# Kernel optimization log

Hardware: AMD Instinct MI355X
Metric: run time of the kernel (lower is better)

The kernel has to match this reference:

```python
import jax, jax.numpy as jnp
import numpy as np

H = 256        # hidden_size
V = 8192       # output_size / vocab
S = 4096       # encoder source length


def _lin(x, w, b):
    # torch nn.Linear: x @ W^T + b, W shape [out, in]
    return x @ w.T + b


def setup_inputs() -> dict:
    key = jax.random.key(0)
    ks = jax.random.split(key, 32)
    f32 = jnp.float32

    def w(i, shape, scale=0.02):
        return (jax.random.normal(ks[i], shape) * scale).astype(f32)

    inp = {
        "input_tok": jax.random.randint(ks[0], (1,), 0, V),
        "hidden": jax.random.normal(ks[1], (1, H), dtype=f32),
        "encoder_outputs": jax.random.normal(ks[2], (S, 2 * H), dtype=f32),
        "emb": w(3, (V, V), 0.02),
        "Uz_w": w(4, (H, V)), "Uz_b": jnp.zeros((H,), f32),
        "Wz_w": w(5, (H, H)), "Wz_b": jnp.zeros((H,), f32),
        "Cz_w": w(6, (H, 2 * H)), "Cz_b": jnp.zeros((H,), f32),
        "Ur_w": w(7, (H, V)), "Ur_b": jnp.zeros((H,), f32),
        "Wr_w": w(8, (H, H)), "Wr_b": jnp.zeros((H,), f32),
        "Cr_w": w(9, (H, 2 * H)), "Cr_b": jnp.zeros((H,), f32),
        "Uh_w": w(10, (H, V)), "Uh_b": jnp.zeros((H,), f32),
        "Wh_w": w(11, (H, H)), "Wh_b": jnp.zeros((H,), f32),
        "Ch_w": w(12, (H, 2 * H)), "Ch_b": jnp.zeros((H,), f32),
        "Ua_w": w(13, (H, 2 * H)), "Ua_b": jnp.zeros((H,), f32),
        "Wa_w": w(14, (H, H)), "Wa_b": jnp.zeros((H,), f32),
        "Va_w": w(15, (1, H)), "Va_b": jnp.zeros((1,), f32),
        "V_w": w(16, (V, H)), "V_b": jnp.zeros((V,), f32),
    }
    return inp


def reference(input_tok, hidden, encoder_outputs, emb,
              Uz_w, Uz_b, Wz_w, Wz_b, Cz_w, Cz_b,
              Ur_w, Ur_b, Wr_w, Wr_b, Cr_w, Cr_b,
              Uh_w, Uh_b, Wh_w, Wh_b, Ch_w, Ch_b,
              Ua_w, Ua_b, Wa_w, Wa_b, Va_w, Va_b,
              V_w, V_b):
    y = emb[input_tok[0]].reshape(1, V)                                   # [1, V]
    # Bahdanau additive attention over encoder states (softmax over dim 0)
    e = jnp.tanh(_lin(hidden, Wa_w, Wa_b) + _lin(encoder_outputs, Ua_w, Ua_b))  # [S, H]
    Eij = _lin(e, Va_w, Va_b)                                             # [S, 1]
    aij = jax.nn.softmax(Eij, axis=0)                                     # [S, 1]
    Ci = jnp.sum(aij * encoder_outputs, axis=0).reshape(1, 2 * H)         # [1, 2H]
    # GRU gates
    z = jax.nn.sigmoid(_lin(y, Uz_w, Uz_b) + _lin(hidden, Wz_w, Wz_b) + _lin(Ci, Cz_w, Cz_b))
    r = jax.nn.sigmoid(_lin(y, Ur_w, Ur_b) + _lin(hidden, Wr_w, Wr_b) + _lin(Ci, Cr_w, Cr_b))
    c = jnp.tanh(_lin(y, Uh_w, Uh_b) + _lin(r * hidden, Wh_w, Wh_b) + _lin(Ci, Ch_w, Ch_b))
    hidden_new = (1.0 - z) * c + z * hidden                               # [1, H]
    out = jax.nn.log_softmax(_lin(hidden_new, V_w, V_b), axis=1)          # [1, V]
    return (out, hidden_new, aij)
```

## Files before the change

### kernel.cpp

```cpp
#include <hip/hip_runtime.h>
#include <hip/hip_bf16.h>

typedef unsigned short u16;
typedef unsigned int u32;

#define HD 256
#define VD 8192
#define SD 4096
#define H2 512

#define WS_FLAG  0
#define WS_WAH   64
#define WS_STATS 320
#define WS_CI    384
#define WS_G     896
#define WS_HN    1664
#define WS_EIJ   2048

__device__ __forceinline__ float bflo(u32 w) { return __uint_as_float(w << 16); }
__device__ __forceinline__ float bfhi(u32 w) { return __uint_as_float(w & 0xffff0000u); }
__device__ __forceinline__ float bfu(u16 u)  { return __uint_as_float(((u32)u) << 16); }

__device__ __forceinline__ float ldf(const void* p, long i, int bf) {
    return bf ? bfu(((const u16*)p)[i]) : ((const float*)p)[i];
}
__device__ __forceinline__ float4 ldf4(const void* p, long i, int bf) {
    if (bf) {
        uint2 u = *(const uint2*)((const u16*)p + i);
        return make_float4(bflo(u.x), bfhi(u.x), bflo(u.y), bfhi(u.y));
    }
    return *(const float4*)((const float*)p + i);
}
__device__ __forceinline__ void stf(void* p, long i, int bf, float v) {
    if (bf) ((__hip_bfloat16*)p)[i] = __float2bfloat16(v);
    else    ((float*)p)[i] = v;
}
__device__ __forceinline__ float dot4(float4 a, float4 b, float acc) {
    acc = fmaf(a.x, b.x, acc); acc = fmaf(a.y, b.y, acc);
    acc = fmaf(a.z, b.z, acc); return fmaf(a.w, b.w, acc);
}

__global__ __launch_bounds__(64) void ks_sniff(const void* emb, int* flag) {
    int t = threadIdx.x;
    const u16* p = (const u16*)emb;
    int ok = 0;
    #pragma unroll
    for (int j = 0; j < 2; ++j) {
        float x = fabsf(bfu(p[2 * (t + 64 * j)]));
        ok += (x == 0.f || (x > 3e-6f && x < 0.25f)) ? 1 : 0;
    }
    #pragma unroll
    for (int o = 32; o; o >>= 1) ok += __shfl_xor(ok, o);
    if (t == 0) flag[0] = (ok >= 96) ? 1 : 0;
}

__global__ __launch_bounds__(256) void k0_wah(const void* Wa_w, const void* Wa_b,
                                              const void* hidden, const int* flag,
                                              float* __restrict__ wa_h) {
    __shared__ __align__(16) float hs[HD];
    int t = threadIdx.x; int bf = flag[0];
    hs[t] = ldf(hidden, t, bf);
    __syncthreads();
    float acc = 0.f;
    for (int k = 0; k < HD; k += 4)
        acc = dot4(ldf4(Wa_w, (long)t * HD + k, bf), *(const float4*)&hs[k], acc);
    wa_h[t] = acc + ldf(Wa_b, t, bf);
}

__global__ __launch_bounds__(256) void k1_scores(const void* enc, const void* Ua_w,
                                                 const void* Ua_b, const void* Va_w,
                                                 const void* Va_b,
                                                 const float* __restrict__ wa_h,
                                                 const int* flag,
                                                 float* __restrict__ Eij) {
    __shared__ __align__(16) float encs[16 * H2];
    int t = threadIdx.x; int bf = flag[0];
    int lane = t & 63, sg = t >> 6;
    int h0 = lane * 4;
    long s0 = (long)blockIdx.x * 16;

    for (int i = t * 4; i < 16 * H2; i += 1024) {
        float4 v = ldf4(enc, s0 * H2 + i, bf);
        *(float4*)&encs[i] = v;
    }
    __syncthreads();

    float acc[4][4];
    #pragma unroll
    for (int a = 0; a < 4; ++a)
        #pragma unroll
        for (int b = 0; b < 4; ++b) acc[a][b] = 0.f;

    for (int kc = 0; kc < H2; kc += 4) {
        float4 a0 = ldf4(Ua_w, (long)(h0 + 0) * H2 + kc, bf);
        float4 a1 = ldf4(Ua_w, (long)(h0 + 1) * H2 + kc, bf);
        float4 a2 = ldf4(Ua_w, (long)(h0 + 2) * H2 + kc, bf);
        float4 a3 = ldf4(Ua_w, (long)(h0 + 3) * H2 + kc, bf);
        #pragma unroll
        for (int ss = 0; ss < 4; ++ss) {
            float4 ev = *(const float4*)&encs[(sg * 4 + ss) * H2 + kc];
            acc[ss][0] = dot4(a0, ev, acc[ss][0]);
            acc[ss][1] = dot4(a1, ev, acc[ss][1]);
            acc[ss][2] = dot4(a2, ev, acc[ss][2]);
            acc[ss][3] = dot4(a3, ev, acc[ss][3]);
        }
    }

    float bias[4], va[4];
    #pragma unroll
    for (int j = 0; j < 4; ++j) {
        bias[j] = wa_h[h0 + j] + ldf(Ua_b, h0 + j, bf);
        va[j]   = ldf(Va_w, h0 + j, bf);
    }
    float vb = ldf(Va_b, 0, bf);
    #pragma unroll
    for (int ss = 0; ss < 4; ++ss) {
        float v = 0.f;
        #pragma unroll
        for (int j = 0; j < 4; ++j)
            v += va[j] * tanhf(acc[ss][j] + bias[j]);
        #pragma unroll
        for (int o = 32; o; o >>= 1) v += __shfl_xor(v, o);
        if (lane == 0) Eij[s0 + sg * 4 + ss] = v + vb;
    }
}

__global__ __launch_bounds__(256) void k2_stats(const float* __restrict__ Eij,
                                                float* __restrict__ stats,
                                                float* __restrict__ Ci) {
    __shared__ float sh[4];
    int t = threadIdx.x, lane = t & 63, wv = t >> 6;
    float m = -1e30f;
    for (int i = t; i < SD; i += 256) m = fmaxf(m, Eij[i]);
    #pragma unroll
    for (int o = 32; o; o >>= 1) m = fmaxf(m, __shfl_xor(m, o));
    if (lane == 0) sh[wv] = m;
    __syncthreads();
    m = fmaxf(fmaxf(sh[0], sh[1]), fmaxf(sh[2], sh[3]));
    __syncthreads();
    float s = 0.f;
    for (int i = t; i < SD; i += 256) s += __expf(Eij[i] - m);
    #pragma unroll
    for (int o = 32; o; o >>= 1) s += __shfl_xor(s, o);
    if (lane == 0) sh[wv] = s;
    __syncthreads();
    s = sh[0] + sh[1] + sh[2] + sh[3];
    if (t == 0) { stats[0] = m; stats[1] = 1.f / s; }
    for (int i = t; i < H2; i += 256) Ci[i] = 0.f;
}

__global__ __launch_bounds__(256) void k3_ci(const float* __restrict__ Eij,
                                             const float* __restrict__ stats,
                                             const void* enc, const int* flag,
                                             void* out, float* __restrict__ Ci) {
    __shared__ float a[64];
    int t = threadIdx.x; int bf = flag[0];
    long s0 = (long)blockIdx.x * 64;
    if (t < 64) {
        float v = __expf(Eij[s0 + t] - stats[0]) * stats[1];
        a[t] = v;
        stf(out, 8448 + s0 + t, bf, v);
    }
    __syncthreads();
    float acc0 = 0.f, acc1 = 0.f;
    for (int s = 0; s < 64; ++s) {
        float av = a[s];
        acc0 = fmaf(av, ldf(enc, (s0 + s) * H2 + t, bf), acc0);
        acc1 = fmaf(av, ldf(enc, (s0 + s) * H2 + t + 256, bf), acc1);
    }
    atomicAdd(Ci + t, acc0);
    atomicAdd(Ci + t + 256, acc1);
}

__global__ __launch_bounds__(256) void k4_gates(const int* __restrict__ tok, const void* emb,
        const void* Uz_w, const void* Uz_b, const void* Wz_w, const void* Wz_b,
        const void* Ur_w, const void* Ur_b, const void* Wr_w, const void* Wr_b,
        const void* Uh_w, const void* Uh_b, const void* hidden,
        const int* flag, float* __restrict__ G) {
    int t = threadIdx.x, lane = t & 63, wv = t >> 6;
    int bf = flag[0];
    int wg = blockIdx.x * 4 + wv;
    int g = wg >> 8, i = wg & 255;
    const void* U = (g == 0 ? Uz_w : (g == 1 ? Ur_w : Uh_w));
    long urow = (long)i * VD;
    long yrow = (long)tok[0] * VD;
    float acc = 0.f;
    for (int c = 0; c < VD; c += 512) {
        long k = c + lane * 8;
        float4 u0 = ldf4(U, urow + k, bf),   u1 = ldf4(U, urow + k + 4, bf);
        float4 y0 = ldf4(emb, yrow + k, bf), y1 = ldf4(emb, yrow + k + 4, bf);
        acc = dot4(u0, y0, acc);
        acc = dot4(u1, y1, acc);
    }
    if (g < 2) {
        const void* W = (g == 0 ? Wz_w : Wr_w);
        long k = (long)lane * 4;
        acc = dot4(ldf4(W, (long)i * HD + k, bf), ldf4(hidden, k, bf), acc);
    }
    #pragma unroll
    for (int o = 32; o; o >>= 1) acc += __shfl_xor(acc, o);
    if (lane == 0) {
        float b;
        if (g == 0)      b = ldf(Uz_b, i, bf) + ldf(Wz_b, i, bf);
        else if (g == 1) b = ldf(Ur_b, i, bf) + ldf(Wr_b, i, bf);
        else             b = ldf(Uh_b, i, bf);
        G[wg] = acc + b;
    }
}

__global__ __launch_bounds__(256) void k5_combine(const float* __restrict__ G,
        const float* __restrict__ Ci,
        const void* Cz_w, const void* Cz_b, const void* Cr_w, const void* Cr_b,
        const void* Wh_w, const void* Wh_b, const void* Ch_w, const void* Ch_b,
        const void* hidden, const int* flag,
        float* __restrict__ hn_f, void* out) {
    __shared__ __align__(16) float Cis[H2];
    __shared__ __align__(16) float rh[HD];
    int t = threadIdx.x; int bf = flag[0];
    Cis[t] = Ci[t]; Cis[t + 256] = Ci[t + 256];
    __syncthreads();
    float h = ldf(hidden, t, bf);
    float az = G[t] + ldf(Cz_b, t, bf);
    float ar = G[256 + t] + ldf(Cr_b, t, bf);
    for (int k = 0; k < H2; k += 4) {
        float4 c4 = *(const float4*)&Cis[k];
        az = dot4(ldf4(Cz_w, (long)t * H2 + k, bf), c4, az);
        ar = dot4(ldf4(Cr_w, (long)t * H2 + k, bf), c4, ar);
    }
    float z = 1.f / (1.f + __expf(-az));
    float r = 1.f / (1.f + __expf(-ar));
    rh[t] = r * h;
    __syncthreads();
    float ac = G[512 + t] + ldf(Wh_b, t, bf) + ldf(Ch_b, t, bf);
    for (int k = 0; k < HD; k += 4)
        ac = dot4(ldf4(Wh_w, (long)t * HD + k, bf), *(const float4*)&rh[k], ac);
    for (int k = 0; k < H2; k += 4)
        ac = dot4(ldf4(Ch_w, (long)t * H2 + k, bf), *(const float4*)&Cis[k], ac);
    float cc = tanhf(ac);
    float hnv = (1.f - z) * cc + z * h;
    hn_f[t] = hnv;
    stf(out, 8192 + t, bf, hnv);
}

__global__ __launch_bounds__(256) void k6_logits(const void* Vw, const void* Vb,
                                                 const float* __restrict__ hn,
                                                 const int* flag, void* out) {
    __shared__ __align__(16) float hs[HD];
    int t = threadIdx.x; int bf = flag[0];
    hs[t] = hn[t];
    __syncthreads();
    long j = (long)blockIdx.x * 256 + t;
    float acc = 0.f;
    for (int k = 0; k < HD; k += 4)
        acc = dot4(ldf4(Vw, j * HD + k, bf), *(const float4*)&hs[k], acc);
    stf(out, j, bf, acc + ldf(Vb, j, bf));
}

__global__ __launch_bounds__(256) void k7_lsm(void* out, const int* flag) {
    __shared__ float sh[4];
    int t = threadIdx.x, lane = t & 63, wv = t >> 6;
    int bf = flag[0];
    float m = -1e30f;
    for (int i = t; i < VD; i += 256) m = fmaxf(m, ldf(out, i, bf));
    #pragma unroll
    for (int o = 32; o; o >>= 1) m = fmaxf(m, __shfl_xor(m, o));
    if (lane == 0) sh[wv] = m;
    __syncthreads();
    m = fmaxf(fmaxf(sh[0], sh[1]), fmaxf(sh[2], sh[3]));
    __syncthreads();
    float s = 0.f;
    for (int i = t; i < VD; i += 256) s += __expf(ldf(out, i, bf) - m);
    #pragma unroll
    for (int o = 32; o; o >>= 1) s += __shfl_xor(s, o);
    if (lane == 0) sh[wv] = s;
    __syncthreads();
    s = sh[0] + sh[1] + sh[2] + sh[3];
    float lse = m + __logf(s);
    for (int i = t; i < VD; i += 256)
        stf(out, i, bf, ldf(out, i, bf) - lse);
}

extern "C" void kernel_launch(void* const* d_in, const int* in_sizes, int n_in,
                              void* d_out, int out_size, void* d_ws, size_t ws_size,
                              hipStream_t stream) {
    const int*  tok    = (const int*)d_in[0];
    const void* hidden = d_in[1];
    const void* enc    = d_in[2];
    const void* emb    = d_in[3];
    const void* Uz_w = d_in[4],  *Uz_b = d_in[5];
    const void* Wz_w = d_in[6],  *Wz_b = d_in[7];
    const void* Cz_w = d_in[8],  *Cz_b = d_in[9];
    const void* Ur_w = d_in[10], *Ur_b = d_in[11];
    const void* Wr_w = d_in[12], *Wr_b = d_in[13];
    const void* Cr_w = d_in[14], *Cr_b = d_in[15];
    const void* Uh_w = d_in[16], *Uh_b = d_in[17];
    const void* Wh_w = d_in[18], *Wh_b = d_in[19];
    const void* Ch_w = d_in[20], *Ch_b = d_in[21];
    const void* Ua_w = d_in[22], *Ua_b = d_in[23];
    const void* Wa_w = d_in[24], *Wa_b = d_in[25];
    const void* Va_w = d_in[26], *Va_b = d_in[27];
    const void* V_w  = d_in[28], *V_b  = d_in[29];

    float* ws     = (float*)d_ws;
    int*   flag   = (int*)(ws + WS_FLAG);
    float* wa_h   = ws + WS_WAH;
    float* stats  = ws + WS_STATS;
    float* Ci     = ws + WS_CI;
    float* G      = ws + WS_G;
    float* hn_f   = ws + WS_HN;
    float* Eij    = ws + WS_EIJ;

    ks_sniff<<<1, 64, 0, stream>>>(emb, flag);
    k0_wah<<<1, 256, 0, stream>>>(Wa_w, Wa_b, hidden, flag, wa_h);
    k4_gates<<<192, 256, 0, stream>>>(tok, emb, Uz_w, Uz_b, Wz_w, Wz_b,
                                      Ur_w, Ur_b, Wr_w, Wr_b, Uh_w, Uh_b,
                                      hidden, flag, G);
    k1_scores<<<256, 256, 0, stream>>>(enc, Ua_w, Ua_b, Va_w, Va_b, wa_h, flag, Eij);
    k2_stats<<<1, 256, 0, stream>>>(Eij, stats, Ci);
    k3_ci<<<64, 256, 0, stream>>>(Eij, stats, enc, flag, d_out, Ci);
    k5_combine<<<1, 256, 0, stream>>>(G, Ci, Cz_w, Cz_b, Cr_w, Cr_b,
                                      Wh_w, Wh_b, Ch_w, Ch_b, hidden, flag,
                                      hn_f, d_out);
    k6_logits<<<32, 256, 0, stream>>>(V_w, V_b, hn_f, flag, d_out);
    k7_lsm<<<1, 256, 0, stream>>>(d_out, flag);
}
```

Baseline: 607.7 us.

## Drop bf16 sniffing, fuse Wa·h into gates, parallelize GRU combine and logits

Removes the runtime dtype-sniff kernel and all bf16/fp32 branching, so every kernel assumes fp32 inputs. The Wa·hidden product runs as an extra block of the gates kernel, which removes one launch. The single-block combine kernel becomes two multi-block kernels (C-projection dots, then the Wh·(r*h) step plus the hidden update), each using one wave per output row. The logits kernel moves to 128 blocks with wave-per-row coalesced loads. This targets serial single-block work and uncoalesced per-thread row reads, at the cost of one extra launch for the combine step.

```diff
diff --git a/kernel.cpp b/kernel.cpp
--- a/kernel.cpp
+++ b/kernel.cpp
@@ -1,7 +1,6 @@
 #include <hip/hip_runtime.h>
 #include <hip/hip_bf16.h>
 
-typedef unsigned short u16;
 typedef unsigned int u32;
 
 #define HD 256
@@ -9,80 +8,84 @@
 #define SD 4096
 #define H2 512
 
-#define WS_FLAG  0
-#define WS_WAH   64
+#define WS_WAH   0
 #define WS_STATS 320
 #define WS_CI    384
 #define WS_G     896
-#define WS_HN    1664
-#define WS_EIJ   2048
-
-__device__ __forceinline__ float bflo(u32 w) { return __uint_as_float(w << 16); }
-__device__ __forceinline__ float bfhi(u32 w) { return __uint_as_float(w & 0xffff0000u); }
-__device__ __forceinline__ float bfu(u16 u)  { return __uint_as_float(((u32)u) << 16); }
-
-__device__ __forceinline__ float ldf(const void* p, long i, int bf) {
-    return bf ? bfu(((const u16*)p)[i]) : ((const float*)p)[i];
-}
-__device__ __forceinline__ float4 ldf4(const void* p, long i, int bf) {
-    if (bf) {
-        uint2 u = *(const uint2*)((const u16*)p + i);
-        return make_float4(bflo(u.x), bfhi(u.x), bflo(u.y), bfhi(u.y));
-    }
-    return *(const float4*)((const float*)p + i);
-}
-__device__ __forceinline__ void stf(void* p, long i, int bf, float v) {
-    if (bf) ((__hip_bfloat16*)p)[i] = __float2bfloat16(v);
-    else    ((float*)p)[i] = v;
-}
+#define WS_AZR   1664
+#define WS_HN    2432
+#define WS_EIJ   2688
+
 __device__ __forceinline__ float dot4(float4 a, float4 b, float acc) {
     acc = fmaf(a.x, b.x, acc); acc = fmaf(a.y, b.y, acc);
     acc = fmaf(a.z, b.z, acc); return fmaf(a.w, b.w, acc);
 }
-
-__global__ __launch_bounds__(64) void ks_sniff(const void* emb, int* flag) {
+__device__ __forceinline__ float wred64(float v) {
+    #pragma unroll
+    for (int o = 32; o; o >>= 1) v += __shfl_xor(v, o);
+    return v;
+}
+
+__global__ __launch_bounds__(256) void ka_gates(const int* __restrict__ tok,
+        const float* __restrict__ emb,
+        const float* __restrict__ Uz_w, const float* __restrict__ Uz_b,
+        const float* __restrict__ Wz_w, const float* __restrict__ Wz_b,
+        const float* __restrict__ Ur_w, const float* __restrict__ Ur_b,
+        const float* __restrict__ Wr_w, const float* __restrict__ Wr_b,
+        const float* __restrict__ Uh_w, const float* __restrict__ Uh_b,
+        const float* __restrict__ Wa_w, const float* __restrict__ Wa_b,
+        const float* __restrict__ hidden,
+        float* __restrict__ G, float* __restrict__ wa_h) {
+    int t = threadIdx.x, lane = t & 63, wv = t >> 6;
+    if (blockIdx.x == 192) {
+        __shared__ __align__(16) float hs[HD];
+        hs[t] = hidden[t];
+        __syncthreads();
+        float acc = 0.f;
+        const float4* row = (const float4*)(Wa_w + (size_t)t * HD);
+        #pragma unroll 4
+        for (int k = 0; k < HD / 4; ++k)
+            acc = dot4(row[k], *(const float4*)&hs[k * 4], acc);
+        wa_h[t] = acc + Wa_b[t];
+        return;
+    }
+    int wg = blockIdx.x * 4 + wv;
+    int g = wg >> 8, i = wg & 255;
+    const float* U = (g == 0 ? Uz_w : (g == 1 ? Ur_w : Uh_w)) + (size_t)i * VD;
+    const float* y = emb + (size_t)tok[0] * VD;
+    float acc = 0.f;
+    for (int c = 0; c < VD; c += 512) {
+        int k = c + lane * 8;
+        acc = dot4(*(const float4*)(U + k),     *(const float4*)(y + k),     acc);
+        acc = dot4(*(const float4*)(U + k + 4), *(const float4*)(y + k + 4), acc);
+    }
+    if (g < 2) {
+        const float* W = (g == 0 ? Wz_w : Wr_w) + (size_t)i * HD;
+        int k = lane * 4;
+        acc = dot4(*(const float4*)(W + k), *(const float4*)(hidden + k), acc);
+    }
+    acc = wred64(acc);
+    if (lane == 0) {
+        float b;
+        if (g == 0)      b = Uz_b[i] + Wz_b[i];
+        else if (g == 1) b = Ur_b[i] + Wr_b[i];
+        else             b = Uh_b[i];
+        G[wg] = acc + b;
+    }
+}
+
+__global__ __launch_bounds__(256) void k1_scores(const float* __restrict__ enc,
+        const float* __restrict__ Ua_w, const float* __restrict__ Ua_b,
+        const float* __restrict__ Va_w, const float* __restrict__ Va_b,
+        const float* __restrict__ wa_h, float* __restrict__ Eij) {
+    __shared__ __align__(16) float encs[16 * H2];
     int t = threadIdx.x;
-    const u16* p = (const u16*)emb;
-    int ok = 0;
-    #pragma unroll
-    for (int j = 0; j < 2; ++j) {
-        float x = fabsf(bfu(p[2 * (t + 64 * j)]));
-        ok += (x == 0.f || (x > 3e-6f && x < 0.25f)) ? 1 : 0;
-    }
-    #pragma unroll
-    for (int o = 32; o; o >>= 1) ok += __shfl_xor(ok, o);
-    if (t == 0) flag[0] = (ok >= 96) ? 1 : 0;
-}
-
-__global__ __launch_bounds__(256) void k0_wah(const void* Wa_w, const void* Wa_b,
-                                              const void* hidden, const int* flag,
-                                              float* __restrict__ wa_h) {
-    __shared__ __align__(16) float hs[HD];
-    int t = threadIdx.x; int bf = flag[0];
-    hs[t] = ldf(hidden, t, bf);
-    __syncthreads();
-    float acc = 0.f;
-    for (int k = 0; k < HD; k += 4)
-        acc = dot4(ldf4(Wa_w, (long)t * HD + k, bf), *(const float4*)&hs[k], acc);
-    wa_h[t] = acc + ldf(Wa_b, t, bf);
-}
-
-__global__ __launch_bounds__(256) void k1_scores(const void* enc, const void* Ua_w,
-                                                 const void* Ua_b, const void* Va_w,
-                                                 const void* Va_b,
-                                                 const float* __restrict__ wa_h,
-                                                 const int* flag,
-                                                 float* __restrict__ Eij) {
-    __shared__ __align__(16) float encs[16 * H2];
-    int t = threadIdx.x; int bf = flag[0];
     int lane = t & 63, sg = t >> 6;
     int h0 = lane * 4;
     long s0 = (long)blockIdx.x * 16;
 
-    for (int i = t * 4; i < 16 * H2; i += 1024) {
-        float4 v = ldf4(enc, s0 * H2 + i, bf);
-        *(float4*)&encs[i] = v;
-    }
+    for (int i = t * 4; i < 16 * H2; i += 1024)
+        *(float4*)&encs[i] = *(const float4*)(enc + s0 * H2 + i);
     __syncthreads();
 
     float acc[4][4];
@@ -91,11 +94,15 @@
         #pragma unroll
         for (int b = 0; b < 4; ++b) acc[a][b] = 0.f;
 
+    const float* r0 = Ua_w + (size_t)(h0 + 0) * H2;
+    const float* r1 = Ua_w + (size_t)(h0 + 1) * H2;
+    const float* r2 = Ua_w + (size_t)(h0 + 2) * H2;
+    const float* r3 = Ua_w + (size_t)(h0 + 3) * H2;
     for (int kc = 0; kc < H2; kc += 4) {
-        float4 a0 = ldf4(Ua_w, (long)(h0 + 0) * H2 + kc, bf);
-        float4 a1 = ldf4(Ua_w, (long)(h0 + 1) * H2 + kc, bf);
-        float4 a2 = ldf4(Ua_w, (long)(h0 + 2) * H2 + kc, bf);
-        float4 a3 = ldf4(Ua_w, (long)(h0 + 3) * H2 + kc, bf);
+        float4 a0 = *(const float4*)(r0 + kc);
+        float4 a1 = *(const float4*)(r1 + kc);
+        float4 a2 = *(const float4*)(r2 + kc);
+        float4 a3 = *(const float4*)(r3 + kc);
         #pragma unroll
         for (int ss = 0; ss < 4; ++ss) {
             float4 ev = *(const float4*)&encs[(sg * 4 + ss) * H2 + kc];
@@ -109,18 +116,17 @@
     float bias[4], va[4];
     #pragma unroll
     for (int j = 0; j < 4; ++j) {
-        bias[j] = wa_h[h0 + j] + ldf(Ua_b, h0 + j, bf);
-        va[j]   = ldf(Va_w, h0 + j, bf);
-    }
-    float vb = ldf(Va_b, 0, bf);
+        bias[j] = wa_h[h0 + j] + Ua_b[h0 + j];
+        va[j]   = Va_w[h0 + j];
+    }
+    float vb = Va_b[0];
     #pragma unroll
     for (int ss = 0; ss < 4; ++ss) {
         float v = 0.f;
         #pragma unroll
         for (int j = 0; j < 4; ++j)
             v += va[j] * tanhf(acc[ss][j] + bias[j]);
-        #pragma unroll
-        for (int o = 32; o; o >>= 1) v += __shfl_xor(v, o);
+        v = wred64(v);
         if (lane == 0) Eij[s0 + sg * 4 + ss] = v + vb;
     }
 }
@@ -140,8 +146,7 @@
     __syncthreads();
     float s = 0.f;
     for (int i = t; i < SD; i += 256) s += __expf(Eij[i] - m);
-    #pragma unroll
-    for (int o = 32; o; o >>= 1) s += __shfl_xor(s, o);
+    s = wred64(s);
     if (lane == 0) sh[wv] = s;
     __syncthreads();
     s = sh[0] + sh[1] + sh[2] + sh[3];
@@ -151,117 +156,96 @@
 
 __global__ __launch_bounds__(256) void k3_ci(const float* __restrict__ Eij,
                                              const float* __restrict__ stats,
-                                             const void* enc, const int* flag,
-                                             void* out, float* __restrict__ Ci) {
+                                             const float* __restrict__ enc,
+                                             float* __restrict__ out,
+                                             float* __restrict__ Ci) {
     __shared__ float a[64];
-    int t = threadIdx.x; int bf = flag[0];
+    int t = threadIdx.x;
     long s0 = (long)blockIdx.x * 64;
     if (t < 64) {
         float v = __expf(Eij[s0 + t] - stats[0]) * stats[1];
         a[t] = v;
-        stf(out, 8448 + s0 + t, bf, v);
+        out[8448 + s0 + t] = v;
     }
     __syncthreads();
     float acc0 = 0.f, acc1 = 0.f;
     for (int s = 0; s < 64; ++s) {
         float av = a[s];
-        acc0 = fmaf(av, ldf(enc, (s0 + s) * H2 + t, bf), acc0);
-        acc1 = fmaf(av, ldf(enc, (s0 + s) * H2 + t + 256, bf), acc1);
+        const float* r = enc + (s0 + s) * H2;
+        acc0 = fmaf(av, r[t], acc0);
+        acc1 = fmaf(av, r[t + 256], acc1);
     }
     atomicAdd(Ci + t, acc0);
     atomicAdd(Ci + t + 256, acc1);
 }
 
-__global__ __launch_bounds__(256) void k4_gates(const int* __restrict__ tok, const void* emb,
-        const void* Uz_w, const void* Uz_b, const void* Wz_w, const void* Wz_b,
-        const void* Ur_w, const void* Ur_b, const void* Wr_w, const void* Wr_b,
-        const void* Uh_w, const void* Uh_b, const void* hidden,
-        const int* flag, float* __restrict__ G) {
-    int t = threadIdx.x, lane = t & 63, wv = t >> 6;
-    int bf = flag[0];
+__global__ __launch_bounds__(256) void k5a_cdots(const float* __restrict__ G,
+        const float* __restrict__ Ci,
+        const float* __restrict__ Cz_w, const float* __restrict__ Cz_b,
+        const float* __restrict__ Cr_w, const float* __restrict__ Cr_b,
+        const float* __restrict__ Ch_w, const float* __restrict__ Ch_b,
+        const float* __restrict__ Wh_b,
+        float* __restrict__ AZR) {
+    int t = threadIdx.x, lane = t & 63, wv = t >> 6;
     int wg = blockIdx.x * 4 + wv;
     int g = wg >> 8, i = wg & 255;
-    const void* U = (g == 0 ? Uz_w : (g == 1 ? Ur_w : Uh_w));
-    long urow = (long)i * VD;
-    long yrow = (long)tok[0] * VD;
-    float acc = 0.f;
-    for (int c = 0; c < VD; c += 512) {
-        long k = c + lane * 8;
-        float4 u0 = ldf4(U, urow + k, bf),   u1 = ldf4(U, urow + k + 4, bf);
-        float4 y0 = ldf4(emb, yrow + k, bf), y1 = ldf4(emb, yrow + k + 4, bf);
-        acc = dot4(u0, y0, acc);
-        acc = dot4(u1, y1, acc);
-    }
-    if (g < 2) {
-        const void* W = (g == 0 ? Wz_w : Wr_w);
-        long k = (long)lane * 4;
-        acc = dot4(ldf4(W, (long)i * HD + k, bf), ldf4(hidden, k, bf), acc);
-    }
-    #pragma unroll
-    for (int o = 32; o; o >>= 1) acc += __shfl_xor(acc, o);
+    const float* C = (g == 0 ? Cz_w : (g == 1 ? Cr_w : Ch_w)) + (size_t)i * H2;
+    int k = lane * 8;
+    float acc = dot4(*(const float4*)(C + k),     *(const float4*)(Ci + k),     0.f);
+    acc = dot4(*(const float4*)(C + k + 4), *(const float4*)(Ci + k + 4), acc);
+    acc = wred64(acc);
     if (lane == 0) {
         float b;
-        if (g == 0)      b = ldf(Uz_b, i, bf) + ldf(Wz_b, i, bf);
-        else if (g == 1) b = ldf(Ur_b, i, bf) + ldf(Wr_b, i, bf);
-        else             b = ldf(Uh_b, i, bf);
-        G[wg] = acc + b;
-    }
-}
-
-__global__ __launch_bounds__(256) void k5_combine(const float* __restrict__ G,
-        const float* __restrict__ Ci,
-        const void* Cz_w, const void* Cz_b, const void* Cr_w, const void* Cr_b,
-        const void* Wh_w, const void* Wh_b, const void* Ch_w, const void* Ch_b,
-        const void* hidden, const int* flag,
-        float* __restrict__ hn_f, void* out) {
-    __shared__ __align__(16) float Cis[H2];
-    __shared__ __align__(16) float rh[HD];
-    int t = threadIdx.x; int bf = flag[0];
-    Cis[t] = Ci[t]; Cis[t + 256] = Ci[t + 256];
-    __syncthreads();
-    float h = ldf(hidden, t, bf);
-    float az = G[t] + ldf(Cz_b, t, bf);
-    float ar = G[256 + t] + ldf(Cr_b, t, bf);
-    for (int k = 0; k < H2; k += 4) {
-        float4 c4 = *(const float4*)&Cis[k];
-        az = dot4(ldf4(Cz_w, (long)t * H2 + k, bf), c4, az);
-        ar = dot4(ldf4(Cr_w, (long)t * H2 + k, bf), c4, ar);
-    }
-    float z = 1.f / (1.f + __expf(-az));
-    float r = 1.f / (1.f + __expf(-ar));
-    rh[t] = r * h;
-    __syncthreads();
-    float ac = G[512 + t] + ldf(Wh_b, t, bf) + ldf(Ch_b, t, bf);
-    for (int k = 0; k < HD; k += 4)
-        ac = dot4(ldf4(Wh_w, (long)t * HD + k, bf), *(const float4*)&rh[k], ac);
-    for (int k = 0; k < H2; k += 4)
-        ac = dot4(ldf4(Ch_w, (long)t * H2 + k, bf), *(const float4*)&Cis[k], ac);
-    float cc = tanhf(ac);
-    float hnv = (1.f - z) * cc + z * h;
-    hn_f[t] = hnv;
-    stf(out, 8192 + t, bf, hnv);
-}
-
-__global__ __launch_bounds__(256) void k6_logits(const void* Vw, const void* Vb,
-                                                 const float* __restrict__ hn,
-                                                 const int* flag, void* out) {
-    __shared__ __align__(16) float hs[HD];
-    int t = threadIdx.x; int bf = flag[0];
-    hs[t] = hn[t];
-    __syncthreads();
-    long j = (long)blockIdx.x * 256 + t;
-    float acc = 0.f;
-    for (int k = 0; k < HD; k += 4)
-        acc = dot4(ldf4(Vw, j * HD + k, bf), *(const float4*)&hs[k], acc);
-    stf(out, j, bf, acc + ldf(Vb, j, bf));
-}
-
-__global__ __launch_bounds__(256) void k7_lsm(void* out, const int* flag) {
+        if (g == 0)      b = Cz_b[i];
+        else if (g == 1) b = Cr_b[i];
+        else             b = Wh_b[i] + Ch_b[i];
+        AZR[wg] = G[wg] + acc + b;
+    }
+}
+
+__global__ __launch_bounds__(256) void k5c_hnew(const float* __restrict__ AZR,
+        const float* __restrict__ Wh_w, const float* __restrict__ hidden,
+        float* __restrict__ hn_f, float* __restrict__ out) {
+    int t = threadIdx.x, lane = t & 63, wv = t >> 6;
+    int i = blockIdx.x * 4 + wv;
+    int k = lane * 4;
+    float4 ar4 = *(const float4*)(AZR + 256 + k);
+    float4 h4  = *(const float4*)(hidden + k);
+    float4 rh;
+    rh.x = h4.x / (1.f + __expf(-ar4.x));
+    rh.y = h4.y / (1.f + __expf(-ar4.y));
+    rh.z = h4.z / (1.f + __expf(-ar4.z));
+    rh.w = h4.w / (1.f + __expf(-ar4.w));
+    float acc = dot4(*(const float4*)(Wh_w + (size_t)i * HD + k), rh, 0.f);
+    acc = wred64(acc);
+    if (lane == 0) {
+        float c = tanhf(AZR[512 + i] + acc);
+        float z = 1.f / (1.f + __expf(-AZR[i]));
+        float hnv = (1.f - z) * c + z * hidden[i];
+        hn_f[i] = hnv;
+        out[8192 + i] = hnv;
+    }
+}
+
+__global__ __launch_bounds__(256) void k6_logits(const float* __restrict__ Vw,
+        const float* __restrict__ Vb, const float* __restrict__ hn,
+        float* __restrict__ out) {
+    int t = threadIdx.x, lane = t & 63, wv = t >> 6;
+    float4 h4 = *(const float4*)(hn + lane * 4);
+    long r0 = ((long)blockIdx.x * 4 + wv) * 16;
+    for (int rr = 0; rr < 16; ++rr) {
+        long j = r0 + rr;
+        float acc = dot4(*(const float4*)(Vw + j * HD + lane * 4), h4, 0.f);
+        acc = wred64(acc);
+        if (lane == 0) out[j] = acc + Vb[j];
+    }
+}
+
+__global__ __launch_bounds__(256) void k7_lsm(float* __restrict__ out) {
     __shared__ float sh[4];
     int t = threadIdx.x, lane = t & 63, wv = t >> 6;
-    int bf = flag[0];
     float m = -1e30f;
-    for (int i = t; i < VD; i += 256) m = fmaxf(m, ldf(out, i, bf));
+    for (int i = t; i < VD; i += 256) m = fmaxf(m, out[i]);
     #pragma unroll
     for (int o = 32; o; o >>= 1) m = fmaxf(m, __shfl_xor(m, o));
     if (lane == 0) sh[wv] = m;
@@ -269,58 +253,55 @@
     m = fmaxf(fmaxf(sh[0], sh[1]), fmaxf(sh[2], sh[3]));
     __syncthreads();
     float s = 0.f;
-    for (int i = t; i < VD; i += 256) s += __expf(ldf(out, i, bf) - m);
-    #pragma unroll
-    for (int o = 32; o; o >>= 1) s += __shfl_xor(s, o);
+    for (int i = t; i < VD; i += 256) s += __expf(out[i] - m);
+    s = wred64(s);
     if (lane == 0) sh[wv] = s;
     __syncthreads();
     s = sh[0] + sh[1] + sh[2] + sh[3];
     float lse = m + __logf(s);
-    for (int i = t; i < VD; i += 256)
-        stf(out, i, bf, ldf(out, i, bf) - lse);
+    for (int i = t; i < VD; i += 256) out[i] = out[i] - lse;
 }
 
 extern "C" void kernel_launch(void* const* d_in, const int* in_sizes, int n_in,
                               void* d_out, int out_size, void* d_ws, size_t ws_size,
                               hipStream_t stream) {
-    const int*  tok    = (const int*)d_in[0];
-    const void* hidden = d_in[1];
-    const void* enc    = d_in[2];
-    const void* emb    = d_in[3];
-    const void* Uz_w = d_in[4],  *Uz_b = d_in[5];
-    const void* Wz_w = d_in[6],  *Wz_b = d_in[7];
-    const void* Cz_w = d_in[8],  *Cz_b = d_in[9];
-    const void* Ur_w = d_in[10], *Ur_b = d_in[11];
-    const void* Wr_w = d_in[12], *Wr_b = d_in[13];
-    const void* Cr_w = d_in[14], *Cr_b = d_in[15];
-    const void* Uh_w = d_in[16], *Uh_b = d_in[17];
-    const void* Wh_w = d_in[18], *Wh_b = d_in[19];
-    const void* Ch_w = d_in[20], *Ch_b = d_in[21];
-    const void* Ua_w = d_in[22], *Ua_b = d_in[23];
-    const void* Wa_w = d_in[24], *Wa_b = d_in[25];
-    const void* Va_w = d_in[26], *Va_b = d_in[27];
-    const void* V_w  = d_in[28], *V_b  = d_in[29];
-
-    float* ws     = (float*)d_ws;
-    int*   flag   = (int*)(ws + WS_FLAG);
-    float* wa_h   = ws + WS_WAH;
-    float* stats  = ws + WS_STATS;
-    float* Ci     = ws + WS_CI;
-    float* G      = ws + WS_G;
-    float* hn_f   = ws + WS_HN;
-    float* Eij    = ws + WS_EIJ;
-
-    ks_sniff<<<1, 64, 0, stream>>>(emb, flag);
-    k0_wah<<<1, 256, 0, stream>>>(Wa_w, Wa_b, hidden, flag, wa_h);
-    k4_gates<<<192, 256, 0, stream>>>(tok, emb, Uz_w, Uz_b, Wz_w, Wz_b,
+    const int*   tok    = (const int*)d_in[0];
+    const float* hidden = (const float*)d_in[1];
+    const float* enc    = (const float*)d_in[2];
+    const float* emb    = (const float*)d_in[3];
+    const float* Uz_w = (const float*)d_in[4],  *Uz_b = (const float*)d_in[5];
+    const float* Wz_w = (const float*)d_in[6],  *Wz_b = (const float*)d_in[7];
+    const float* Cz_w = (const float*)d_in[8],  *Cz_b = (const float*)d_in[9];
+    const float* Ur_w = (const float*)d_in[10], *Ur_b = (const float*)d_in[11];
+    const float* Wr_w = (const float*)d_in[12], *Wr_b = (const float*)d_in[13];
+    const float* Cr_w = (const float*)d_in[14], *Cr_b = (const float*)d_in[15];
+    const float* Uh_w = (const float*)d_in[16], *Uh_b = (const float*)d_in[17];
+    const float* Wh_w = (const float*)d_in[18], *Wh_b = (const float*)d_in[19];
+    const float* Ch_w = (const float*)d_in[20], *Ch_b = (const float*)d_in[21];
+    const float* Ua_w = (const float*)d_in[22], *Ua_b = (const float*)d_in[23];
+    const float* Wa_w = (const float*)d_in[24], *Wa_b = (const float*)d_in[25];
+    const float* Va_w = (const float*)d_in[26], *Va_b = (const float*)d_in[27];
+    const float* V_w  = (const float*)d_in[28], *V_b  = (const float*)d_in[29];
+
+    float* ws    = (float*)d_ws;
+    float* wa_h  = ws + WS_WAH;
+    float* stats = ws + WS_STATS;
+    float* Ci    = ws + WS_CI;
+    float* G     = ws + WS_G;
+    float* AZR   = ws + WS_AZR;
+    float* hn_f  = ws + WS_HN;
+    float* Eij   = ws + WS_EIJ;
+    float* out   = (float*)d_out;
+
+    ka_gates<<<193, 256, 0, stream>>>(tok, emb, Uz_w, Uz_b, Wz_w, Wz_b,
                                       Ur_w, Ur_b, Wr_w, Wr_b, Uh_w, Uh_b,
-                                      hidden, flag, G);
-    k1_scores<<<256, 256, 0, stream>>>(enc, Ua_w, Ua_b, Va_w, Va_b, wa_h, flag, Eij);
+                                      Wa_w, Wa_b, hidden, G, wa_h);
+    k1_scores<<<256, 256, 0, stream>>>(enc, Ua_w, Ua_b, Va_w, Va_b, wa_h, Eij);
     k2_stats<<<1, 256, 0, stream>>>(Eij, stats, Ci);
-    k3_ci<<<64, 256, 0, stream>>>(Eij, stats, enc, flag, d_out, Ci);
-    k5_combine<<<1, 256, 0, stream>>>(G, Ci, Cz_w, Cz_b, Cr_w, Cr_b,
-                                      Wh_w, Wh_b, Ch_w, Ch_b, hidden, flag,
-                                      hn_f, d_out);
-    k6_logits<<<32, 256, 0, stream>>>(V_w, V_b, hn_f, flag, d_out);
-    k7_lsm<<<1, 256, 0, stream>>>(d_out, flag);
-}
+    k3_ci<<<64, 256, 0, stream>>>(Eij, stats, enc, out, Ci);
+    k5a_cdots<<<192, 256, 0, stream>>>(G, Ci, Cz_w, Cz_b, Cr_w, Cr_b,
+                                       Ch_w, Ch_b, Wh_b, AZR);
+    k5c_hnew<<<64, 256, 0, stream>>>(AZR, Wh_w, hidden, hn_f, out);
+    k6_logits<<<128, 256, 0, stream>>>(V_w, V_b, hn_f, out);
+    k7_lsm<<<1, 256, 0, stream>>>(out);
+}
```

After: 493.5 us. -18.8%, faster.
